# Optimization experiments

Measured on AMD Instinct MI355X. Metric: run time of the kernel, lower is better.

## Reference

```python
import jax, jax.numpy as jnp
import numpy as np

MX, SX = 0.0, 1.0  # msx
MY, SY = 0.0, 1.0  # msy


def _mode_linear(inp, phase, w, b):
    # Equivalent to: w_p = einsum('ji,imk->jmk', phase, w); out = squeeze(inp[:,None,:] @ w_p) + phase @ b
    # Fused blended form avoids the (batch, in, out) per-sample weight intermediate.
    out = jnp.einsum('bd,idh,bi->bh', inp, w, phase)
    return out + phase @ b


def setup_inputs() -> dict:
    key = jax.random.key(0)
    ks = jax.random.split(key, 4)
    B, D_IN, H, D_OUT = 32768, 256, 1024, 64
    x = jax.random.normal(ks[0], (B, D_IN + 2), dtype=jnp.float32)
    w1 = jax.random.normal(ks[1], (2, D_IN, H), dtype=jnp.float32) * 0.05
    b1 = jnp.zeros((2, H), dtype=jnp.float32)
    w2 = jax.random.normal(ks[2], (2, H, H), dtype=jnp.float32) * 0.05
    b2 = jnp.zeros((2, H), dtype=jnp.float32)
    w3 = jax.random.normal(ks[3], (2, H, D_OUT), dtype=jnp.float32) * 0.05
    b3 = jnp.zeros((2, D_OUT), dtype=jnp.float32)
    return {"x": x, "w1": w1, "b1": b1, "w2": w2, "b2": b2, "w3": w3, "b3": b3}


def reference(x, w1, b1, w2, b2, w3, b3):
    phase = x[:, -2:]                 # unscaled phase weights, per original code
    xs = (x - MX) / SX
    h = xs[:, :-2]                    # [B, D_IN]
    out = jax.nn.elu(_mode_linear(h, phase, w1, b1))
    out = jax.nn.elu(_mode_linear(out, phase, w2, b2))
    out = _mode_linear(out, phase, w3, b3)
    return out * SY + MY
```

## Files before the change

### kernel.cpp

```cpp
#include <hip/hip_runtime.h>

typedef unsigned short u16;
typedef __bf16 bf16x8 __attribute__((ext_vector_type(8)));
typedef float f32x4 __attribute__((ext_vector_type(4)));

#define AS1 __attribute__((address_space(1)))
#define AS3 __attribute__((address_space(3)))

static __device__ __forceinline__ u16 f2bf(float f) {
  union { float f; unsigned u; } v; v.f = f;
  unsigned r = (v.u + 0x7fff + ((v.u >> 16) & 1)) >> 16;
  return (u16)r;
}

__global__ void prep_x_kernel(const float* __restrict__ x, u16* __restrict__ hx,
                              float2* __restrict__ phase, int B) {
  int i = blockIdx.x * blockDim.x + threadIdx.x;
  int total = B * 128;
  if (i < total) {
    int row = i >> 7, k2 = (i & 127);
    const float2 v = *reinterpret_cast<const float2*>(x + (size_t)row * 258 + k2 * 2);
    u16 a = f2bf(v.x), b = f2bf(v.y);
    *reinterpret_cast<unsigned*>(hx + (size_t)row * 256 + k2 * 2) =
        (unsigned)a | ((unsigned)b << 16);
  }
  if (i < B) {
    phase[i] = *reinterpret_cast<const float2*>(x + (size_t)i * 258 + 256);
  }
}

__global__ void prep_w_kernel(const float* __restrict__ w, u16* __restrict__ wt,
                              int K, int N) {
  __shared__ u16 tile[64][65];
  int k0 = blockIdx.x * 64, n0 = blockIdx.y * 64, mode = blockIdx.z;
  const float* src = w + (size_t)mode * K * N;
  u16* dst = wt + (size_t)mode * N * K;
  int c = threadIdx.x & 63;
  int r4 = threadIdx.x >> 6;
#pragma unroll
  for (int i = 0; i < 16; ++i) {
    int r = r4 + i * 4;
    tile[r][c] = f2bf(src[(size_t)(k0 + r) * N + n0 + c]);
  }
  __syncthreads();
#pragma unroll
  for (int i = 0; i < 16; ++i) {
    int r = r4 + i * 4;
    dst[(size_t)(n0 + r) * K + k0 + c] = tile[c][r];
  }
}

__global__ void prep_w_int_kernel(const float* __restrict__ w, u16* __restrict__ wt,
                                  int K, int N) {
  __shared__ u16 tile[64][65];
  int k0 = blockIdx.x * 64, n0 = blockIdx.y * 64, mode = blockIdx.z;
  const float* src = w + (size_t)mode * K * N;
  int c = threadIdx.x & 63;
  int r4 = threadIdx.x >> 6;
#pragma unroll
  for (int i = 0; i < 16; ++i) {
    int r = r4 + i * 4;
    tile[r][c] = f2bf(src[(size_t)(k0 + r) * N + n0 + c]);
  }
  __syncthreads();
#pragma unroll
  for (int i = 0; i < 16; ++i) {
    int n = n0 + r4 + i * 4;
    int np = ((n >> 4) << 5) + (mode << 4) + (n & 15);
    wt[(size_t)np * K + k0 + c] = tile[c][r4 + i * 4];
  }
}

template <bool ELU_STORE>
__global__ __launch_bounds__(512, 2) void gemm8p(
    const u16* __restrict__ A, const u16* __restrict__ Wt,
    const float* __restrict__ bias, const float2* __restrict__ phase,
    u16* __restrict__ out, int K, int Np) {
  __shared__ u16 lds[2][2][16384];
  const int tnc = Np >> 8;
  const int nwg = gridDim.x;
  int id = blockIdx.x;
  const int cpx = nwg >> 3;
  id = (id & 7) * cpx + (id >> 3);
  const int m0 = (id / tnc) * 256;
  const int n0 = (id % tnc) * 256;
  const int t = threadIdx.x;
  const int lane = t & 63;
  const int wave = t >> 6;
  const int wr = wave >> 2, wc = wave & 3;
  const int lr = lane & 15, ks = lane >> 4;
  const int cswz = lr * 64 + ((((ks * 8) ^ (((lane >> 3) & 1) << 4))) << 1);

  int soff[4];
#pragma unroll
  for (int ld = 0; ld < 4; ++ld) {
    int e = (ld * 512 + t) * 8;
    int cp8 = e & 31;
    int rl = (e >> 5) & 15;
    int st = e >> 9;
    int r = ((st >> 1) << 4) + rl;
    int c0 = ((st & 1) << 5) + (cp8 ^ (((rl >> 3) & 1) << 4));
    soff[ld] = r * K + c0;
  }
  const u16* Abase = A + (size_t)m0 * K;
  const u16* Bbase = Wt + (size_t)n0 * K;

  f32x4 acc[8][4] = {};
  const int NT = K >> 6;

  auto stage = [&](int bb, int kt) {
#pragma unroll
    for (int ld = 0; ld < 4; ++ld)
      __builtin_amdgcn_global_load_lds(
          (const AS1 void*)(Abase + kt + soff[ld]),
          (AS3 void*)(&lds[bb][0][(ld * 512 + t) * 8]), 16, 0, 0);
#pragma unroll
    for (int ld = 0; ld < 4; ++ld)
      __builtin_amdgcn_global_load_lds(
          (const AS1 void*)(Bbase + kt + soff[ld]),
          (AS3 void*)(&lds[bb][1][(ld * 512 + t) * 8]), 16, 0, 0);
  };

#define BAR()                         \
  asm volatile("" ::: "memory");      \
  __builtin_amdgcn_s_barrier();       \
  asm volatile("" ::: "memory");

  stage(0, 0);
  asm volatile("s_waitcnt vmcnt(0)" ::: "memory");
  BAR();

  for (int tt = 0; tt < NT; ++tt) {
    const int b = tt & 1;
    const char* lA = (const char*)&lds[b][0][0];
    const char* lB = (const char*)&lds[b][1][0];
    bf16x8 af[4][2], bfr[2][2];

#define LOADA(mh)                                                             \
  _Pragma("unroll") for (int m = 0; m < 4; ++m)                               \
  _Pragma("unroll") for (int kk = 0; kk < 2; ++kk)                            \
      af[m][kk] = *(const bf16x8*)(lA +                                       \
          ((((wr * 8 + (mh)*4 + m) * 2 + kk) << 10) + cswz));
#define LOADB(nh)                                                             \
  _Pragma("unroll") for (int n = 0; n < 2; ++n)                               \
  _Pragma("unroll") for (int kk = 0; kk < 2; ++kk)                            \
      bfr[n][kk] = *(const bf16x8*)(lB +                                      \
          ((((wc * 4 + (nh)*2 + n) * 2 + kk) << 10) + cswz));
#define MFMAQ(mh, nh)                                                         \
  __builtin_amdgcn_s_setprio(1);                                              \
  _Pragma("unroll") for (int m = 0; m < 4; ++m)                               \
  _Pragma("unroll") for (int n = 0; n < 2; ++n)                               \
  _Pragma("unroll") for (int kk = 0; kk < 2; ++kk)                            \
      acc[(mh)*4 + m][(nh)*2 + n] = __builtin_amdgcn_mfma_f32_16x16x32_bf16(  \
          af[m][kk], bfr[n][kk], acc[(mh)*4 + m][(nh)*2 + n], 0, 0, 0);       \
  __builtin_amdgcn_s_setprio(0);

    LOADA(0); LOADB(0);
    if (tt + 1 < NT) stage(b ^ 1, (tt + 1) << 6);
    BAR();
    __builtin_amdgcn_sched_barrier(0);
    MFMAQ(0, 0);
    BAR();
    LOADB(1);
    BAR();
    __builtin_amdgcn_sched_barrier(0);
    MFMAQ(0, 1);
    BAR();
    LOADA(1);
    BAR();
    __builtin_amdgcn_sched_barrier(0);
    MFMAQ(1, 1);
    BAR();
    LOADB(0);
    BAR();
    __builtin_amdgcn_sched_barrier(0);
    MFMAQ(1, 0);
    asm volatile("s_waitcnt vmcnt(0)" ::: "memory");
    BAR();
#undef LOADA
#undef LOADB
#undef MFMAQ
  }

  const int Nreal = Np >> 1;
  const int colbase = (n0 + wc * 64) >> 1;
  float bias0[2], bias1[2];
#pragma unroll
  for (int pj = 0; pj < 2; ++pj) {
    int ncol = colbase + pj * 16 + lr;
    bias0[pj] = bias[ncol];
    bias1[pj] = bias[Nreal + ncol];
  }
#pragma unroll
  for (int m = 0; m < 8; ++m) {
#pragma unroll
    for (int j = 0; j < 4; ++j) {
      int grow = m0 + wr * 128 + m * 16 + ks * 4 + j;
      float2 ph = phase[grow];
#pragma unroll
      for (int pj = 0; pj < 2; ++pj) {
        int ncol = colbase + pj * 16 + lr;
        float v = ph.x * (acc[m][pj * 2 + 0][j] + bias0[pj]) +
                  ph.y * (acc[m][pj * 2 + 1][j] + bias1[pj]);
        if (ELU_STORE) v = v > 0.f ? v : (__expf(v) - 1.f);
        out[(size_t)grow * Nreal + ncol] = f2bf(v);
      }
    }
  }
#undef BAR
}

template <int BM, int BN, int WM, int WN, bool ELU_BF16>
__launch_bounds__(256, 2) __global__
void gemm_dualmode(const u16* __restrict__ A, const u16* __restrict__ WT,
                   const float* __restrict__ bias, const float2* __restrict__ phase,
                   void* __restrict__ out, int K, int N) {
  constexpr int MF = WM / 16, NF = WN / 16;
  __shared__ u16 ldsA[BM * 32];
  __shared__ u16 ldsB[2][BN * 32];
  const int m0 = blockIdx.x * BM;
  const int n0 = blockIdx.y * BN;
  const int t = threadIdx.x;
  const int wave = t >> 6, lane = t & 63;
  constexpr int NWC = BN / WN;
  const int wr = wave / NWC, wc = wave % NWC;
  const int lr = lane & 15, ks = lane >> 4;

  f32x4 acc[2][MF][NF] = {};

  for (int kt = 0; kt < K; kt += 32) {
#pragma unroll
    for (int i = 0; i < BM / 64; ++i) {
      int tt = t + i * 256;
      int r = tt >> 2, c8 = (tt & 3) * 8;
      __builtin_amdgcn_global_load_lds(
          (const AS1 void*)(A + (size_t)(m0 + r) * K + kt + c8),
          (AS3 void*)(ldsA + (size_t)tt * 8), 16, 0, 0);
    }
#pragma unroll
    for (int md = 0; md < 2; ++md) {
#pragma unroll
      for (int i = 0; i < BN / 64; ++i) {
        int tt = t + i * 256;
        int r = tt >> 2, c8 = (tt & 3) * 8;
        __builtin_amdgcn_global_load_lds(
            (const AS1 void*)(WT + (size_t)md * N * K + (size_t)(n0 + r) * K + kt + c8),
            (AS3 void*)(ldsB[md] + (size_t)tt * 8), 16, 0, 0);
      }
    }
    __syncthreads();

    bf16x8 af[MF], b0f[NF], b1f[NF];
#pragma unroll
    for (int m = 0; m < MF; ++m)
      af[m] = *reinterpret_cast<const bf16x8*>(&ldsA[(wr * WM + m * 16 + lr) * 32 + ks * 8]);
#pragma unroll
    for (int n = 0; n < NF; ++n) {
      b0f[n] = *reinterpret_cast<const bf16x8*>(&ldsB[0][(wc * WN + n * 16 + lr) * 32 + ks * 8]);
      b1f[n] = *reinterpret_cast<const bf16x8*>(&ldsB[1][(wc * WN + n * 16 + lr) * 32 + ks * 8]);
    }
#pragma unroll
    for (int m = 0; m < MF; ++m) {
#pragma unroll
      for (int n = 0; n < NF; ++n) {
        acc[0][m][n] = __builtin_amdgcn_mfma_f32_16x16x32_bf16(af[m], b0f[n], acc[0][m][n], 0, 0, 0);
        acc[1][m][n] = __builtin_amdgcn_mfma_f32_16x16x32_bf16(af[m], b1f[n], acc[1][m][n], 0, 0, 0);
      }
    }
    __syncthreads();
  }

#pragma unroll
  for (int m = 0; m < MF; ++m) {
#pragma unroll
    for (int j = 0; j < 4; ++j) {
      int grow = m0 + wr * WM + m * 16 + ks * 4 + j;
      float2 ph = phase[grow];
#pragma unroll
      for (int n = 0; n < NF; ++n) {
        int gcol = n0 + wc * WN + n * 16 + lr;
        float v = ph.x * (acc[0][m][n][j] + bias[gcol]) +
                  ph.y * (acc[1][m][n][j] + bias[N + gcol]);
        if (ELU_BF16) {
          v = v > 0.f ? v : (__expf(v) - 1.f);
          ((u16*)out)[(size_t)grow * N + gcol] = f2bf(v);
        } else {
          ((float*)out)[(size_t)grow * N + gcol] = v;
        }
      }
    }
  }
}

extern "C" void kernel_launch(void* const* d_in, const int* in_sizes, int n_in,
                              void* d_out, int out_size, void* d_ws, size_t ws_size,
                              hipStream_t stream) {
  const float* x  = (const float*)d_in[0];
  const float* w1 = (const float*)d_in[1];
  const float* b1 = (const float*)d_in[2];
  const float* w2 = (const float*)d_in[3];
  const float* b2 = (const float*)d_in[4];
  const float* w3 = (const float*)d_in[5];
  const float* b3 = (const float*)d_in[6];
  float* out = (float*)d_out;
  const int B = 32768, DIN = 256, H = 1024, DOUT = 64;

  char* ws = (char*)d_ws;
  u16* W1Ti = (u16*)ws;    ws += (size_t)2 * H * DIN * 2;
  u16* W2Ti = (u16*)ws;    ws += (size_t)2 * H * H * 2;
  u16* W3T = (u16*)ws;     ws += (size_t)2 * DOUT * H * 2;
  float2* phase = (float2*)ws; ws += (size_t)B * 8;
  u16* hx = (u16*)ws;      ws += (size_t)B * DIN * 2;
  u16* h1 = (u16*)ws;      ws += (size_t)B * H * 2;
  u16* h2 = (u16*)ws;      ws += (size_t)B * H * 2;

  prep_x_kernel<<<(B * 128 + 255) / 256, 256, 0, stream>>>(x, hx, phase, B);
  prep_w_int_kernel<<<dim3(DIN / 64, H / 64, 2), 256, 0, stream>>>(w1, W1Ti, DIN, H);
  prep_w_int_kernel<<<dim3(H / 64, H / 64, 2), 256, 0, stream>>>(w2, W2Ti, H, H);
  prep_w_kernel<<<dim3(H / 64, DOUT / 64, 2), 256, 0, stream>>>(w3, W3T, H, DOUT);

  const int nwg = (B / 256) * (2 * H / 256);
  gemm8p<true><<<nwg, 512, 0, stream>>>(hx, W1Ti, b1, phase, h1, DIN, 2 * H);
  gemm8p<true><<<nwg, 512, 0, stream>>>(h1, W2Ti, b2, phase, h2, H, 2 * H);
  gemm_dualmode<128, 64, 64, 32, false>
      <<<dim3(B / 128, DOUT / 64), 256, 0, stream>>>(h2, W3T, b3, phase, out, H, DOUT);
}
```

Before: 240.6 us.

## Replace double-buffered K=64 GEMM with four-stage K=32 LDS ring pipeline

The main bf16 GEMM moves from two LDS buffers of K=64 tiles to a four-slot ring of K=32 tiles. Three tiles are prefetched ahead, and each wait uses vmcnt(8) instead of draining all loads. The goal is to keep more global-to-LDS traffic in flight and hide memory latency behind MFMA work. In exchange there are twice as many loop iterations and barriers per unit of K, and fewer MFMAs between synchronisations.

```diff
diff --git a/kernel.cpp b/kernel.cpp
--- a/kernel.cpp
+++ b/kernel.cpp
@@ -72,11 +72,11 @@
 }
 
 template <bool ELU_STORE>
-__global__ __launch_bounds__(512, 2) void gemm8p(
+__global__ __launch_bounds__(512, 2) void gemm_ring(
     const u16* __restrict__ A, const u16* __restrict__ Wt,
     const float* __restrict__ bias, const float2* __restrict__ phase,
     u16* __restrict__ out, int K, int Np) {
-  __shared__ u16 lds[2][2][16384];
+  __shared__ u16 lds[4][2][8192];
   const int tnc = Np >> 8;
   const int nwg = gridDim.x;
   int id = blockIdx.x;
@@ -89,98 +89,84 @@
   const int wave = t >> 6;
   const int wr = wave >> 2, wc = wave & 3;
   const int lr = lane & 15, ks = lane >> 4;
-  const int cswz = lr * 64 + ((((ks * 8) ^ (((lane >> 3) & 1) << 4))) << 1);
-
-  int soff[4];
-#pragma unroll
-  for (int ld = 0; ld < 4; ++ld) {
+  const int cswz = lr * 64 + (((ks * 8) ^ ((lr >> 3) << 4)) << 1);
+
+  int soff[2];
+#pragma unroll
+  for (int ld = 0; ld < 2; ++ld) {
     int e = (ld * 512 + t) * 8;
-    int cp8 = e & 31;
+    int st = e >> 9;
     int rl = (e >> 5) & 15;
-    int st = e >> 9;
-    int r = ((st >> 1) << 4) + rl;
-    int c0 = ((st & 1) << 5) + (cp8 ^ (((rl >> 3) & 1) << 4));
-    soff[ld] = r * K + c0;
+    int c = e & 31;
+    int c0 = c ^ (((rl >> 3) & 1) << 4);
+    soff[ld] = (st * 16 + rl) * K + c0;
   }
   const u16* Abase = A + (size_t)m0 * K;
   const u16* Bbase = Wt + (size_t)n0 * K;
 
   f32x4 acc[8][4] = {};
-  const int NT = K >> 6;
-
-  auto stage = [&](int bb, int kt) {
-#pragma unroll
-    for (int ld = 0; ld < 4; ++ld)
+  const int NT = K >> 5;
+
+  auto stage = [&](int bb, int tile) {
+    const int kt = tile << 5;
+#pragma unroll
+    for (int ld = 0; ld < 2; ++ld)
       __builtin_amdgcn_global_load_lds(
           (const AS1 void*)(Abase + kt + soff[ld]),
           (AS3 void*)(&lds[bb][0][(ld * 512 + t) * 8]), 16, 0, 0);
 #pragma unroll
-    for (int ld = 0; ld < 4; ++ld)
+    for (int ld = 0; ld < 2; ++ld)
       __builtin_amdgcn_global_load_lds(
           (const AS1 void*)(Bbase + kt + soff[ld]),
           (AS3 void*)(&lds[bb][1][(ld * 512 + t) * 8]), 16, 0, 0);
   };
 
-#define BAR()                         \
-  asm volatile("" ::: "memory");      \
-  __builtin_amdgcn_s_barrier();       \
+#define BAR()                    \
+  asm volatile("" ::: "memory"); \
+  __builtin_amdgcn_s_barrier();  \
   asm volatile("" ::: "memory");
 
+#define LOADA(mh)                                 \
+  _Pragma("unroll") for (int m = 0; m < 4; ++m)   \
+      af[m] = *(const bf16x8*)(lA + (((wr * 8 + (mh)*4 + m) << 10) + cswz));
+#define LOADB()                                   \
+  _Pragma("unroll") for (int n = 0; n < 4; ++n)   \
+      bfr[n] = *(const bf16x8*)(lB + (((wc * 4 + n) << 10) + cswz));
+#define MFMAH(mh)                                                       \
+  __builtin_amdgcn_s_setprio(1);                                        \
+  _Pragma("unroll") for (int m = 0; m < 4; ++m)                         \
+  _Pragma("unroll") for (int n = 0; n < 4; ++n)                         \
+      acc[(mh)*4 + m][n] = __builtin_amdgcn_mfma_f32_16x16x32_bf16(     \
+          af[m], bfr[n], acc[(mh)*4 + m][n], 0, 0, 0);                  \
+  __builtin_amdgcn_s_setprio(0);
+
   stage(0, 0);
-  asm volatile("s_waitcnt vmcnt(0)" ::: "memory");
+  stage(1, 1);
+  stage(2, 2);
+  asm volatile("s_waitcnt vmcnt(8)" ::: "memory");
   BAR();
 
   for (int tt = 0; tt < NT; ++tt) {
-    const int b = tt & 1;
-    const char* lA = (const char*)&lds[b][0][0];
-    const char* lB = (const char*)&lds[b][1][0];
-    bf16x8 af[4][2], bfr[2][2];
-
-#define LOADA(mh)                                                             \
-  _Pragma("unroll") for (int m = 0; m < 4; ++m)                               \
-  _Pragma("unroll") for (int kk = 0; kk < 2; ++kk)                            \
-      af[m][kk] = *(const bf16x8*)(lA +                                       \
-          ((((wr * 8 + (mh)*4 + m) * 2 + kk) << 10) + cswz));
-#define LOADB(nh)                                                             \
-  _Pragma("unroll") for (int n = 0; n < 2; ++n)                               \
-  _Pragma("unroll") for (int kk = 0; kk < 2; ++kk)                            \
-      bfr[n][kk] = *(const bf16x8*)(lB +                                      \
-          ((((wc * 4 + (nh)*2 + n) * 2 + kk) << 10) + cswz));
-#define MFMAQ(mh, nh)                                                         \
-  __builtin_amdgcn_s_setprio(1);                                              \
-  _Pragma("unroll") for (int m = 0; m < 4; ++m)                               \
-  _Pragma("unroll") for (int n = 0; n < 2; ++n)                               \
-  _Pragma("unroll") for (int kk = 0; kk < 2; ++kk)                            \
-      acc[(mh)*4 + m][(nh)*2 + n] = __builtin_amdgcn_mfma_f32_16x16x32_bf16(  \
-          af[m][kk], bfr[n][kk], acc[(mh)*4 + m][(nh)*2 + n], 0, 0, 0);       \
-  __builtin_amdgcn_s_setprio(0);
-
-    LOADA(0); LOADB(0);
-    if (tt + 1 < NT) stage(b ^ 1, (tt + 1) << 6);
+    const char* lA = (const char*)&lds[tt & 3][0][0];
+    const char* lB = (const char*)&lds[tt & 3][1][0];
+    bf16x8 af[4], bfr[4];
+    LOADA(0);
+    LOADB();
+    if (tt + 3 < NT) stage((tt + 3) & 3, tt + 3);
     BAR();
     __builtin_amdgcn_sched_barrier(0);
-    MFMAQ(0, 0);
-    BAR();
-    LOADB(1);
-    BAR();
-    __builtin_amdgcn_sched_barrier(0);
-    MFMAQ(0, 1);
+    MFMAH(0);
     BAR();
     LOADA(1);
     BAR();
     __builtin_amdgcn_sched_barrier(0);
-    MFMAQ(1, 1);
+    MFMAH(1);
+    asm volatile("s_waitcnt vmcnt(8)" ::: "memory");
     BAR();
-    LOADB(0);
-    BAR();
-    __builtin_amdgcn_sched_barrier(0);
-    MFMAQ(1, 0);
-    asm volatile("s_waitcnt vmcnt(0)" ::: "memory");
-    BAR();
+  }
 #undef LOADA
 #undef LOADB
-#undef MFMAQ
-  }
+#undef MFMAH
 
   const int Nreal = Np >> 1;
   const int colbase = (n0 + wc * 64) >> 1;
@@ -320,8 +306,8 @@
   prep_w_kernel<<<dim3(H / 64, DOUT / 64, 2), 256, 0, stream>>>(w3, W3T, H, DOUT);
 
   const int nwg = (B / 256) * (2 * H / 256);
-  gemm8p<true><<<nwg, 512, 0, stream>>>(hx, W1Ti, b1, phase, h1, DIN, 2 * H);
-  gemm8p<true><<<nwg, 512, 0, stream>>>(h1, W2Ti, b2, phase, h2, H, 2 * H);
+  gemm_ring<true><<<nwg, 512, 0, stream>>>(hx, W1Ti, b1, phase, h1, DIN, 2 * H);
+  gemm_ring<true><<<nwg, 512, 0, stream>>>(h1, W2Ti, b2, phase, h2, H, 2 * H);
   gemm_dualmode<128, 64, 64, 32, false>
       <<<dim3(B / 128, DOUT / 64), 256, 0, stream>>>(h2, W3T, b3, phase, out, H, DOUT);
 }
```

Measured after the change: 239.7 us. About the same (-0.4%).
